# Optimization experiments

Measured on AMD Instinct MI355X. Metric: run time of the kernel, lower is better.

Reference implementation:

```python
import jax, jax.numpy as jnp
import numpy as np

D_MODEL = 1024
N_HEADS = 16
HEAD_DIM = D_MODEL // N_HEADS
NEG = -10000.0  # module uses -10000, not -inf


def setup_inputs() -> dict:
    key = jax.random.key(0)
    ks = jax.random.split(key, 8)
    B, T = 4, 2048
    q = jax.random.normal(ks[0], (B, T, D_MODEL), dtype=jnp.float32)
    k = jax.random.normal(ks[1], (B, T, D_MODEL), dtype=jnp.float32)
    v = jax.random.normal(ks[2], (B, T, D_MODEL), dtype=jnp.float32)
    attn_mask = jnp.ones((B, T), dtype=jnp.float32)
    # xavier_uniform for square [d, d] weights: limit = sqrt(6/(d+d))
    lim = float(np.sqrt(6.0 / (D_MODEL + D_MODEL)))
    Wq = jax.random.uniform(ks[3], (D_MODEL, D_MODEL), jnp.float32, -lim, lim)
    Wk = jax.random.uniform(ks[4], (D_MODEL, D_MODEL), jnp.float32, -lim, lim)
    Wv = jax.random.uniform(ks[5], (D_MODEL, D_MODEL), jnp.float32, -lim, lim)
    Wo = jax.random.uniform(ks[6], (D_MODEL, D_MODEL), jnp.float32, -lim, lim)
    return {"q": q, "k": k, "v": v, "attn_mask": attn_mask,
            "Wq": Wq, "Wk": Wk, "Wv": Wv, "Wo": Wo, "mask_future": 1}


def _split_heads(x):
    B, T, _ = x.shape
    return x.reshape(B, T, N_HEADS, HEAD_DIM).transpose(0, 2, 1, 3)  # [B,H,T,D]


def reference(q, k, v, attn_mask, Wq, Wk, Wv, Wo, mask_future):
    # torch Linear: y = x @ W.T  (weights stored [out, in])
    qh = _split_heads(jnp.einsum('btd,ed->bte', q, Wq))
    kh = _split_heads(jnp.einsum('btd,ed->bte', k, Wk))
    vh = _split_heads(jnp.einsum('btd,ed->bte', v, Wv))
    L, S = qh.shape[-2], kh.shape[-2]
    # dual scale: each of q and k scaled by 1/d**0.25
    scale = 1.0 / jnp.sqrt(jnp.sqrt(jnp.float32(HEAD_DIM)))
    scores = jnp.einsum('bhld,bhsd->bhls', qh * scale, kh * scale)
    if mask_future:
        causal_bias = jnp.triu(jnp.full((L, S), NEG, dtype=scores.dtype), k=1)
        scores = scores + causal_bias
    # padding mask: attn_mask [B, S] -> broadcast [B,1,1,S]; 0 entries -> -10000
    pad = attn_mask[:, None, None, :]
    scores = jnp.where(pad == 0, jnp.asarray(NEG, scores.dtype), scores)
    probs = jax.nn.softmax(scores, axis=-1)  # dropout p=0.0 -> identity
    ctx = jnp.einsum('bhls,bhsd->bhld', probs, vh)
    B = ctx.shape[0]
    ctx = ctx.transpose(0, 2, 1, 3).reshape(B, L, D_MODEL)
    return jnp.einsum('btd,ed->bte', ctx, Wo)
```

## Files before the change

kernel.cpp:

```cpp
#include <hip/hip_runtime.h>

typedef unsigned short u16;
typedef __attribute__((ext_vector_type(8))) _Float16 f16x8;
typedef __attribute__((ext_vector_type(2))) __fp16 fp16v2;
typedef __attribute__((ext_vector_type(4))) float f32x4;
typedef __attribute__((ext_vector_type(16))) float f32x16;

#define T_SEQ 2048
#define NH 16
#define DH 64
#define DM 1024
#define NEG2 (-14426.95f)
#define QS2 (0.42466089f)

__device__ __forceinline__ unsigned pk2(float a, float b) {
  union { fp16v2 v; unsigned u; } c;
  c.v = __builtin_amdgcn_cvt_pkrtz(a, b);
  return c.u;
}
__device__ __forceinline__ u16 f2h(float a) {
  union { _Float16 h; u16 u; } c; c.h = (_Float16)a; return c.u;
}

__device__ __forceinline__ void async_load16(const void* g, void* l) {
  __builtin_amdgcn_global_load_lds(
      (const __attribute__((address_space(1))) unsigned int*)(g),
      (__attribute__((address_space(3))) unsigned int*)(l), 16, 0, 0);
}

__global__ __launch_bounds__(256) void convert_all(
    const float* __restrict__ q, const float* __restrict__ k, const float* __restrict__ v,
    const float* __restrict__ Wq, const float* __restrict__ Wk, const float* __restrict__ Wv,
    const float* __restrict__ Wo, u16* __restrict__ xb, u16* __restrict__ wb) {
  int blk = blockIdx.x;
  const float* src; u16* dst;
  if (blk < 12288) {
    int s = blk >> 12;
    src = (s == 0) ? q : (s == 1) ? k : v;
    dst = xb + (size_t)s * 8388608u;
    blk &= 4095;
  } else {
    int s = (blk - 12288) >> 9;
    src = (s == 0) ? Wq : (s == 1) ? Wk : (s == 2) ? Wv : Wo;
    dst = wb + (size_t)s * 1048576u;
    blk = (blk - 12288) & 511;
  }
  size_t base = (size_t)blk * 2048 + (size_t)threadIdx.x * 8;
  float4 a = *(const float4*)(src + base);
  float4 b2 = *(const float4*)(src + base + 4);
  uint4 st;
  st.x = pk2(a.x, a.y); st.y = pk2(a.z, a.w);
  st.z = pk2(b2.x, b2.y); st.w = pk2(b2.z, b2.w);
  *(uint4*)(dst + base) = st;
}

__global__ __launch_bounds__(512) void gemm_qkv(const u16* __restrict__ A,
                                                const u16* __restrict__ Wqb,
                                                const u16* __restrict__ Wkb,
                                                const u16* __restrict__ Wvb,
                                                u16* __restrict__ Qh, u16* __restrict__ Kh,
                                                u16* __restrict__ VTh) {
  __shared__ char lds[73728];
  const int tid = threadIdx.x;
  const int wid = tid >> 6, lane = tid & 63;
  const int l32 = lane & 31, lh = lane >> 5;
  const int m0 = blockIdx.x * 256;
  const int n0 = blockIdx.y * 128;
  const int which = n0 >> 10;
  const int n0l = n0 & 1023;
  const u16* As = A + (size_t)which * 8388608u;
  const u16* Bw = (which == 0) ? Wqb : (which == 1) ? Wkb : Wvb;
  f32x16 acc[2][2] = {};

  const u16* gsrc[3]; int ldso[3];
#pragma unroll
  for (int u = 0; u < 3; ++u) {
    int c = wid * 3 + u;
    ldso[u] = c * 1024;
    if (c < 16)
      gsrc[u] = As + (size_t)(m0 + (c >> 1) * 32 + l32) * 1024 + (c & 1) * 16 + lh * 8;
    else {
      int cw = c - 16;
      gsrc[u] = Bw + (size_t)(n0l + (cw >> 1) * 32 + l32) * 1024 + (cw & 1) * 16 + lh * 8;
    }
  }

  const int rOff = (which < 2) ? 16384 : 0;
  const int cOff = 16384 - rOff;
  const int rgo = (which < 2) ? ((wid & 1) * 2) : ((wid >> 1) * 2);
  const int cgo = (which < 2) ? ((wid >> 1) * 2) : ((wid & 1) * 2);

#pragma unroll
  for (int u = 0; u < 3; ++u) async_load16(gsrc[u] + 0 * 32, lds + 0 * 24576 + ldso[u]);
#pragma unroll
  for (int u = 0; u < 3; ++u) async_load16(gsrc[u] + 1 * 32, lds + 1 * 24576 + ldso[u]);

  int slotc = 0, slotn = 2;
  for (int kt = 0; kt < 32; ++kt) {
    if (kt < 31) asm volatile("s_waitcnt vmcnt(3)" ::: "memory");
    else         asm volatile("s_waitcnt vmcnt(0)" ::: "memory");
    __builtin_amdgcn_s_barrier();
    asm volatile("" ::: "memory");
    char* bufc = lds + slotc * 24576;
    if (kt < 30) {
      char* bufn = lds + slotn * 24576;
      int ko = (kt + 2) * 32;
#pragma unroll
      for (int u = 0; u < 3; ++u) async_load16(gsrc[u] + ko, bufn + ldso[u]);
    }
    const char* rb = bufc + rOff;
    const char* cb = bufc + cOff;
    f16x8 r0[2], c0[2], r1[2], c1[2];
#pragma unroll
    for (int i = 0; i < 2; ++i) {
      r0[i] = *(const f16x8*)(rb + ((rgo + i) * 2 + 0) * 1024 + lane * 16);
      c0[i] = *(const f16x8*)(cb + ((cgo + i) * 2 + 0) * 1024 + lane * 16);
    }
#pragma unroll
    for (int i = 0; i < 2; ++i) {
      r1[i] = *(const f16x8*)(rb + ((rgo + i) * 2 + 1) * 1024 + lane * 16);
      c1[i] = *(const f16x8*)(cb + ((cgo + i) * 2 + 1) * 1024 + lane * 16);
    }
    __builtin_amdgcn_s_setprio(1);
#pragma unroll
    for (int i = 0; i < 2; ++i)
#pragma unroll
      for (int j = 0; j < 2; ++j)
        acc[i][j] = __builtin_amdgcn_mfma_f32_32x32x16_f16(r0[i], c0[j], acc[i][j], 0, 0, 0);
#pragma unroll
    for (int i = 0; i < 2; ++i)
#pragma unroll
      for (int j = 0; j < 2; ++j)
        acc[i][j] = __builtin_amdgcn_mfma_f32_32x32x16_f16(r1[i], c1[j], acc[i][j], 0, 0, 0);
    __builtin_amdgcn_s_setprio(0);
    slotc = (slotc == 2) ? 0 : slotc + 1;
    slotn = (slotn == 2) ? 0 : slotn + 1;
  }

  const float s = (which < 2) ? QS2 : 1.0f;
  const int b = m0 >> 11, t0 = m0 & 2047, h0 = n0l >> 6;
  __syncthreads();
  if (which < 2) {
#pragma unroll
    for (int i = 0; i < 2; ++i)
#pragma unroll
      for (int j = 0; j < 2; ++j) {
        int colb = (wid >> 1) * 64 + j * 32 + l32;
        int rowb = (wid & 1) * 64 + i * 32 + 4 * lh;
#pragma unroll
        for (int g = 0; g < 4; ++g) {
          uint2 pv;
          pv.x = pk2(acc[i][j][4 * g + 0] * s, acc[i][j][4 * g + 1] * s);
          pv.y = pk2(acc[i][j][4 * g + 2] * s, acc[i][j][4 * g + 3] * s);
          *(uint2*)(lds + colb * 264 + (rowb + 8 * g) * 2) = pv;
        }
      }
    __syncthreads();
    u16* O = which ? Kh : Qh;
#pragma unroll
    for (int p = 0; p < 8; ++p) {
      int row = p * 32 + (tid >> 4);
      int seg = tid & 15;
      uint4 val = *(const uint4*)(lds + row * 264 + seg * 16);
      int hl = seg >> 3, dh0 = (seg & 7) * 8;
      *(uint4*)(O + (((size_t)(b * NH + h0 + hl) * T_SEQ + t0 + row) << 6) + dh0) = val;
    }
  } else {
#pragma unroll
    for (int i = 0; i < 2; ++i)
#pragma unroll
      for (int j = 0; j < 2; ++j) {
        int colb = (wid & 1) * 64 + j * 32 + l32;
        int rowb = (wid >> 1) * 64 + i * 32 + 4 * lh;
#pragma unroll
        for (int g = 0; g < 4; ++g) {
          uint2 pv;
          pv.x = pk2(acc[i][j][4 * g + 0], acc[i][j][4 * g + 1]);
          pv.y = pk2(acc[i][j][4 * g + 2], acc[i][j][4 * g + 3]);
          *(uint2*)(lds + colb * 520 + (rowb + 8 * g) * 2) = pv;
        }
      }
    __syncthreads();
#pragma unroll
    for (int p = 0; p < 8; ++p) {
      int row = p * 16 + (tid >> 5);
      int seg = tid & 31;
      uint4 val = *(const uint4*)(lds + row * 520 + seg * 16);
      int h = h0 + (row >> 6), dh = row & 63;
      *(uint4*)(VTh + (((size_t)(b * NH + h) * DH + dh) << 11) + t0 + seg * 8) = val;
    }
  }
}

__global__ __launch_bounds__(512) void gemm_out(const u16* __restrict__ A,
                                                const u16* __restrict__ Bw,
                                                float* __restrict__ O) {
  __shared__ char lds[73728];
  const int tid = threadIdx.x;
  const int wid = tid >> 6, lane = tid & 63;
  const int l32 = lane & 31, lh = lane >> 5;
  const int m0 = blockIdx.x * 256, n0 = blockIdx.y * 128;
  f32x16 acc[2][2] = {};

  const u16* gsrc[3]; int ldso[3];
#pragma unroll
  for (int u = 0; u < 3; ++u) {
    int c = wid * 3 + u;
    ldso[u] = c * 1024;
    if (c < 16)
      gsrc[u] = A + (size_t)(m0 + (c >> 1) * 32 + l32) * 1024 + (c & 1) * 16 + lh * 8;
    else {
      int cw = c - 16;
      gsrc[u] = Bw + (size_t)(n0 + (cw >> 1) * 32 + l32) * 1024 + (cw & 1) * 16 + lh * 8;
    }
  }
  const int rgo = (wid >> 1) * 2, cgo = (wid & 1) * 2;

#pragma unroll
  for (int u = 0; u < 3; ++u) async_load16(gsrc[u] + 0 * 32, lds + 0 * 24576 + ldso[u]);
#pragma unroll
  for (int u = 0; u < 3; ++u) async_load16(gsrc[u] + 1 * 32, lds + 1 * 24576 + ldso[u]);

  int slotc = 0, slotn = 2;
  for (int kt = 0; kt < 32; ++kt) {
    if (kt < 31) asm volatile("s_waitcnt vmcnt(3)" ::: "memory");
    else         asm volatile("s_waitcnt vmcnt(0)" ::: "memory");
    __builtin_amdgcn_s_barrier();
    asm volatile("" ::: "memory");
    char* bufc = lds + slotc * 24576;
    if (kt < 30) {
      char* bufn = lds + slotn * 24576;
      int ko = (kt + 2) * 32;
#pragma unroll
      for (int u = 0; u < 3; ++u) async_load16(gsrc[u] + ko, bufn + ldso[u]);
    }
    const char* rb = bufc;
    const char* cb = bufc + 16384;
    f16x8 r0[2], c0[2], r1[2], c1[2];
#pragma unroll
    for (int i = 0; i < 2; ++i) {
      r0[i] = *(const f16x8*)(rb + ((rgo + i) * 2 + 0) * 1024 + lane * 16);
      c0[i] = *(const f16x8*)(cb + ((cgo + i) * 2 + 0) * 1024 + lane * 16);
    }
#pragma unroll
    for (int i = 0; i < 2; ++i) {
      r1[i] = *(const f16x8*)(rb + ((rgo + i) * 2 + 1) * 1024 + lane * 16);
      c1[i] = *(const f16x8*)(cb + ((cgo + i) * 2 + 1) * 1024 + lane * 16);
    }
    __builtin_amdgcn_s_setprio(1);
#pragma unroll
    for (int i = 0; i < 2; ++i)
#pragma unroll
      for (int j = 0; j < 2; ++j)
        acc[i][j] = __builtin_amdgcn_mfma_f32_32x32x16_f16(r0[i], c0[j], acc[i][j], 0, 0, 0);
#pragma unroll
    for (int i = 0; i < 2; ++i)
#pragma unroll
      for (int j = 0; j < 2; ++j)
        acc[i][j] = __builtin_amdgcn_mfma_f32_32x32x16_f16(r1[i], c1[j], acc[i][j], 0, 0, 0);
    __builtin_amdgcn_s_setprio(0);
    slotc = (slotc == 2) ? 0 : slotc + 1;
    slotn = (slotn == 2) ? 0 : slotn + 1;
  }
#pragma unroll
  for (int i = 0; i < 2; ++i)
#pragma unroll
    for (int j = 0; j < 2; ++j) {
      int col = n0 + (wid & 1) * 64 + j * 32 + l32;
      int rowb = m0 + (wid >> 1) * 64 + i * 32 + 4 * lh;
#pragma unroll
      for (int g = 0; g < 4; ++g)
#pragma unroll
        for (int rr = 0; rr < 4; ++rr)
          O[(size_t)(rowb + 8 * g + rr) * 1024 + col] = acc[i][j][4 * g + rr];
    }
}

__global__ __launch_bounds__(512) void attn_kernel(const u16* __restrict__ Qh,
                                                   const u16* __restrict__ Kh,
                                                   const u16* __restrict__ VTh,
                                                   const float* __restrict__ attn_mask,
                                                   const int* __restrict__ mfp,
                                                   u16* __restrict__ ctx) {
  __shared__ char kls[2][8192];
  __shared__ char vls[2][8192];
  __shared__ char pls[8][2048];
  __shared__ int mzf;

  const int tid = threadIdx.x;
  const int wid = tid >> 6, lane = tid & 63;
  const int lm = lane & 15, lq = lane >> 4;
  const int bid = blockIdx.x;
  const int bh_i = bid & 63;
  const int qt = 15 - (bid >> 6);
  const int b = bh_i >> 4, h = bh_i & 15;
  const int mf = *mfp;
  const size_t bh = (size_t)(b * NH + h);
  const u16* Qbh = Qh + bh * T_SEQ * DH;
  const u16* Kbh = Kh + bh * T_SEQ * DH;
  const u16* VTbh = VTh + bh * DH * T_SEQ;
  const float* amb = attn_mask + (size_t)b * T_SEQ;

  f16x8 onev;
#pragma unroll
  for (int i = 0; i < 8; ++i) onev[i] = (_Float16)1.0f;

  if (tid == 0) mzf = 0;
  __syncthreads();
  {
    int az = 0;
    for (int i = tid; i < T_SEQ; i += 512) az |= (amb[i] == 0.0f);
    if (az) mzf = 1;
  }
  __syncthreads();
  const int maskzero = mzf;

  const int qw = qt * 128 + wid * 16;
  f16x8 qf[2];
  qf[0] = *(const f16x8*)(Qbh + (size_t)(qw + lm) * DH + lq * 8);
  qf[1] = *(const f16x8*)(Qbh + (size_t)(qw + lm) * DH + 32 + lq * 8);

  f32x4 acc[4] = {};
  f32x4 accs = {};
  float mprev = -1e30f;

  const int nch = mf ? (qt + 1) * 2 : 32;
  {
    async_load16(Kbh + (size_t)((wid >> 1) * 16 + lm) * DH + (wid & 1) * 32 + lq * 8,
                 kls[0] + wid * 1024);
    async_load16(VTbh + (size_t)((wid >> 1) * 16 + lm) * T_SEQ + (wid & 1) * 32 + lq * 8,
                 vls[0] + wid * 1024);
  }
  for (int c = 0; c < nch; ++c) {
    const int s0 = c * 64;
    asm volatile("s_waitcnt vmcnt(0)" ::: "memory");
    __builtin_amdgcn_s_barrier();
    asm volatile("" ::: "memory");
    if (c + 1 < nch) {
      const int s1 = s0 + 64;
      async_load16(Kbh + (size_t)(s1 + (wid >> 1) * 16 + lm) * DH + (wid & 1) * 32 + lq * 8,
                   kls[(c + 1) & 1] + wid * 1024);
      async_load16(VTbh + (size_t)((wid >> 1) * 16 + lm) * T_SEQ + s1 + (wid & 1) * 32 + lq * 8,
                   vls[(c + 1) & 1] + wid * 1024);
    }
    const char* kcur = kls[c & 1];
    const char* vcur = vls[c & 1];

    f32x4 sc[4];
    for (int st = 0; st < 4; ++st) {
      f32x4 z = {0.f, 0.f, 0.f, 0.f};
      sc[st] = z;
      for (int kk = 0; kk < 2; ++kk) {
        f16x8 kf = *(const f16x8*)(kcur + ((st * 2 + kk) * 64 + lane) * 16);
        sc[st] = __builtin_amdgcn_mfma_f32_16x16x32_f16(kf, qf[kk], sc[st], 0, 0, 0);
      }
    }
    if (maskzero) {
      for (int st = 0; st < 4; ++st) {
        f32x4 mb = *(const f32x4*)(amb + s0 + st * 16 + lq * 4);
        for (int r = 0; r < 4; ++r)
          if (mb[r] == 0.0f) sc[st][r] += NEG2;
      }
    }
    if (mf && (s0 + 64 > qw)) {
      int qg = qw + lm;
      for (int st = 0; st < 4; ++st)
        for (int r = 0; r < 4; ++r)
          if (s0 + st * 16 + lq * 4 + r > qg) sc[st][r] = NEG2;
    }
    float u0 = fmaxf(fmaxf(sc[0][0], sc[0][1]), sc[0][2]);
    float u1 = fmaxf(fmaxf(sc[0][3], sc[1][0]), sc[1][1]);
    float u2 = fmaxf(fmaxf(sc[1][2], sc[1][3]), sc[2][0]);
    float u3 = fmaxf(fmaxf(sc[2][1], sc[2][2]), sc[2][3]);
    float u4 = fmaxf(fmaxf(sc[3][0], sc[3][1]), sc[3][2]);
    float mx = fmaxf(fmaxf(fmaxf(u0, u1), u2), fmaxf(fmaxf(u3, u4), sc[3][3]));
    mx = fmaxf(mx, __shfl_xor(mx, 16));
    mx = fmaxf(mx, __shfl_xor(mx, 32));
    if (__ballot(mx > mprev + 8.0f) != 0ull) {
      float mn2 = fmaxf(mprev, mx);
      float alpha = exp2f(mprev - mn2);
      for (int r = 0; r < 4; ++r) {
        float ar = __shfl(alpha, lq * 4 + r);
        for (int nt = 0; nt < 4; ++nt) acc[nt][r] *= ar;
        accs[r] *= ar;
      }
      mprev = mn2;
    }
    for (int st = 0; st < 4; ++st)
      for (int r = 0; r < 4; ++r)
        sc[st][r] = exp2f(sc[st][r] - mprev);
    {
      char* pw = pls[wid];
      for (int st = 0; st < 4; ++st) {
        int kk = st >> 1;
        int lqp = (st & 1) * 2 + (lq >> 1);
        uint2 pv;
        pv.x = pk2(sc[st][0], sc[st][1]);
        pv.y = pk2(sc[st][2], sc[st][3]);
        *(uint2*)(pw + kk * 1024 + (lqp * 16 + lm) * 16 + (lq & 1) * 8) = pv;
      }
    }
    asm volatile("s_waitcnt lgkmcnt(0)" ::: "memory");
    for (int kk = 0; kk < 2; ++kk) {
      f16x8 pf = *(const f16x8*)(pls[wid] + kk * 1024 + lane * 16);
      for (int nt = 0; nt < 4; ++nt) {
        f16x8 vf = *(const f16x8*)(vcur + ((nt * 2 + kk) * 64 + lane) * 16);
        acc[nt] = __builtin_amdgcn_mfma_f32_16x16x32_f16(pf, vf, acc[nt], 0, 0, 0);
      }
      accs = __builtin_amdgcn_mfma_f32_16x16x32_f16(pf, onev, accs, 0, 0, 0);
    }
  }
  for (int r = 0; r < 4; ++r) {
    float ir = 1.0f / accs[r];
    int t = qw + lq * 4 + r;
    for (int nt = 0; nt < 4; ++nt)
      ctx[((size_t)(b * T_SEQ + t) * DM) + h * DH + nt * 16 + lm] = f2h(acc[nt][r] * ir);
  }
}

extern "C" void kernel_launch(void* const* d_in, const int* in_sizes, int n_in,
                              void* d_out, int out_size, void* d_ws, size_t ws_size,
                              hipStream_t stream) {
  const float* q = (const float*)d_in[0];
  const float* k = (const float*)d_in[1];
  const float* v = (const float*)d_in[2];
  const float* attn_mask = (const float*)d_in[3];
  const float* Wq = (const float*)d_in[4];
  const float* Wk = (const float*)d_in[5];
  const float* Wv = (const float*)d_in[6];
  const float* Wo = (const float*)d_in[7];
  const int* mf = (const int*)d_in[8];

  u16* ws = (u16*)d_ws;
  u16* qb  = ws;
  u16* wqb = ws + 3u * 8388608u;
  u16* wkb = wqb + 1048576u;
  u16* wvb = wkb + 1048576u;
  u16* wob = wvb + 1048576u;
  u16* Qh  = wob + 1048576u;
  u16* Kh  = Qh + 8388608u;
  u16* VTh = Kh + 8388608u;
  u16* ctxb = ws;

  convert_all<<<14336, 256, 0, stream>>>(q, k, v, Wq, Wk, Wv, Wo, qb, wqb);

  dim3 gq(32, 24);
  gemm_qkv<<<gq, 512, 0, stream>>>(qb, wqb, wkb, wvb, Qh, Kh, VTh);

  attn_kernel<<<1024, 512, 0, stream>>>(Qh, Kh, VTh, attn_mask, mf, ctxb);

  dim3 gg(32, 8);
  gemm_out<<<gg, 512, 0, stream>>>(ctxb, wob, (float*)d_out);
}
```

Before: 331.6 us.

## Single-buffer V tile loaded per chunk and halve P staging buffer

Moves the V tile load from double-buffered prefetch into the current iteration, overlapping it with the QK^T and softmax work, and waits on it with a partial vmcnt. The P staging buffer is cut to one 16x32 slice that is written and consumed twice per chunk. Together these shrink LDS use per block, which may allow more blocks per CU. The cost is that V latency is no longer hidden a whole iteration ahead. The reused P slice also adds an extra write/read round trip.

```diff
diff --git a/kernel.cpp b/kernel.cpp
--- a/kernel.cpp
+++ b/kernel.cpp
@@ -283,8 +283,8 @@
                                                    const int* __restrict__ mfp,
                                                    u16* __restrict__ ctx) {
   __shared__ char kls[2][8192];
-  __shared__ char vls[2][8192];
-  __shared__ char pls[8][2048];
+  __shared__ char vls[8192];
+  __shared__ char pls[8][1024];
   __shared__ int mzf;
 
   const int tid = threadIdx.x;
@@ -325,26 +325,21 @@
   float mprev = -1e30f;
 
   const int nch = mf ? (qt + 1) * 2 : 32;
-  {
-    async_load16(Kbh + (size_t)((wid >> 1) * 16 + lm) * DH + (wid & 1) * 32 + lq * 8,
-                 kls[0] + wid * 1024);
-    async_load16(VTbh + (size_t)((wid >> 1) * 16 + lm) * T_SEQ + (wid & 1) * 32 + lq * 8,
-                 vls[0] + wid * 1024);
-  }
+  async_load16(Kbh + (size_t)((wid >> 1) * 16 + lm) * DH + (wid & 1) * 32 + lq * 8,
+               kls[0] + wid * 1024);
+
   for (int c = 0; c < nch; ++c) {
     const int s0 = c * 64;
     asm volatile("s_waitcnt vmcnt(0)" ::: "memory");
     __builtin_amdgcn_s_barrier();
     asm volatile("" ::: "memory");
+    async_load16(VTbh + (size_t)((wid >> 1) * 16 + lm) * T_SEQ + s0 + (wid & 1) * 32 + lq * 8,
+                 vls + wid * 1024);
     if (c + 1 < nch) {
-      const int s1 = s0 + 64;
-      async_load16(Kbh + (size_t)(s1 + (wid >> 1) * 16 + lm) * DH + (wid & 1) * 32 + lq * 8,
+      async_load16(Kbh + (size_t)(s0 + 64 + (wid >> 1) * 16 + lm) * DH + (wid & 1) * 32 + lq * 8,
                    kls[(c + 1) & 1] + wid * 1024);
-      async_load16(VTbh + (size_t)((wid >> 1) * 16 + lm) * T_SEQ + s1 + (wid & 1) * 32 + lq * 8,
-                   vls[(c + 1) & 1] + wid * 1024);
     }
     const char* kcur = kls[c & 1];
-    const char* vcur = vls[c & 1];
 
     f32x4 sc[4];
     for (int st = 0; st < 4; ++st) {
@@ -389,22 +384,43 @@
     for (int st = 0; st < 4; ++st)
       for (int r = 0; r < 4; ++r)
         sc[st][r] = exp2f(sc[st][r] - mprev);
+
     {
       char* pw = pls[wid];
-      for (int st = 0; st < 4; ++st) {
-        int kk = st >> 1;
+      for (int st = 0; st < 2; ++st) {
         int lqp = (st & 1) * 2 + (lq >> 1);
         uint2 pv;
         pv.x = pk2(sc[st][0], sc[st][1]);
         pv.y = pk2(sc[st][2], sc[st][3]);
-        *(uint2*)(pw + kk * 1024 + (lqp * 16 + lm) * 16 + (lq & 1) * 8) = pv;
-      }
-    }
+        *(uint2*)(pw + (lqp * 16 + lm) * 16 + (lq & 1) * 8) = pv;
+      }
+    }
+    if (c + 1 < nch) asm volatile("s_waitcnt vmcnt(1)" ::: "memory");
+    else             asm volatile("s_waitcnt vmcnt(0)" ::: "memory");
     asm volatile("s_waitcnt lgkmcnt(0)" ::: "memory");
-    for (int kk = 0; kk < 2; ++kk) {
-      f16x8 pf = *(const f16x8*)(pls[wid] + kk * 1024 + lane * 16);
+    {
+      f16x8 pf = *(const f16x8*)(pls[wid] + lane * 16);
       for (int nt = 0; nt < 4; ++nt) {
-        f16x8 vf = *(const f16x8*)(vcur + ((nt * 2 + kk) * 64 + lane) * 16);
+        f16x8 vf = *(const f16x8*)(vls + ((nt * 2 + 0) * 64 + lane) * 16);
+        acc[nt] = __builtin_amdgcn_mfma_f32_16x16x32_f16(pf, vf, acc[nt], 0, 0, 0);
+      }
+      accs = __builtin_amdgcn_mfma_f32_16x16x32_f16(pf, onev, accs, 0, 0, 0);
+    }
+    {
+      char* pw = pls[wid];
+      for (int st = 2; st < 4; ++st) {
+        int lqp = (st & 1) * 2 + (lq >> 1);
+        uint2 pv;
+        pv.x = pk2(sc[st][0], sc[st][1]);
+        pv.y = pk2(sc[st][2], sc[st][3]);
+        *(uint2*)(pw + (lqp * 16 + lm) * 16 + (lq & 1) * 8) = pv;
+      }
+    }
+    asm volatile("s_waitcnt lgkmcnt(0)" ::: "memory");
+    {
+      f16x8 pf = *(const f16x8*)(pls[wid] + lane * 16);
+      for (int nt = 0; nt < 4; ++nt) {
+        f16x8 vf = *(const f16x8*)(vls + ((nt * 2 + 1) * 64 + lane) * 16);
         acc[nt] = __builtin_amdgcn_mfma_f32_16x16x32_f16(pf, vf, acc[nt], 0, 0, 0);
       }
       accs = __builtin_amdgcn_mfma_f32_16x16x32_f16(pf, onev, accs, 0, 0, 0);
```

New measurement: 328.0 us. No clear change (-1.1%).
